# Kernel tuning notes

Measured on AMD Instinct MI355X. Metric: run time of the kernel, lower is better.

Reference implementation:

```python
import jax, jax.numpy as jnp
import numpy as np

V, N, K, D, H = 100000, 20000, 32, 256, 256


def setup_inputs() -> dict:
    key = jax.random.key(0)
    k1, k2, k3, k4, k5, k6 = jax.random.split(key, 6)
    return {
        "embed_table": jax.random.normal(k1, (V, D), dtype=jnp.float32),
        "node_ids": jax.random.randint(k2, (N,), 0, V, dtype=jnp.int64) if jax.config.jax_enable_x64 else jax.random.randint(k2, (N,), 0, V, dtype=jnp.int32),
        "nb_ids": jax.random.randint(k3, (N, K), 0, V, dtype=jnp.int32),
        "self_weight": jax.random.normal(k4, (D, H), dtype=jnp.float32) / np.sqrt(D),
        "nb_weight": jax.random.normal(k5, (D, H), dtype=jnp.float32) / np.sqrt(D),
        "bias": jax.random.normal(k6, (2 * H,), dtype=jnp.float32),
    }


def reference(embed_table, node_ids, nb_ids, self_weight, nb_weight, bias):
    # gather self embeddings: [N, D]
    self_attr = embed_table[node_ids]
    # gather sampled neighbor embeddings [N, K, D] and mean-pool over K
    nb_attr = jnp.mean(embed_table[nb_ids], axis=1)
    from_self = self_attr @ self_weight          # [N, H]
    from_nb = nb_attr @ nb_weight                # [N, H]
    out = jnp.concatenate((from_self, from_nb), axis=1) + bias  # concat combine
    return jax.nn.relu(out)
```

## Files before the change

### kernel.cpp

```cpp
#include <hip/hip_runtime.h>

#define VV 100000
#define NN 20000
#define KK 32
#define DD 256
#define HH 256
#define BN 16

typedef __attribute__((ext_vector_type(8))) short bf16x8;
typedef __attribute__((ext_vector_type(4))) float f32x4;

__device__ __forceinline__ ushort f2bf(float f) {
    uint u = __float_as_uint(f);
    return (ushort)((u + 0x7FFFu + ((u >> 16) & 1u)) >> 16);
}
__device__ __forceinline__ float bf2f(ushort u) {
    return __uint_as_float(((uint)u) << 16);
}

__global__ __launch_bounds__(256) void k_conv(
    const float* __restrict__ E, ushort* __restrict__ Eb)
{
    const size_t i = ((size_t)blockIdx.x * 256 + threadIdx.x) * 8;
    const f32x4 a = __builtin_nontemporal_load((const f32x4*)&E[i]);
    const f32x4 b = __builtin_nontemporal_load((const f32x4*)&E[i + 4]);
    bf16x8 v;
    v[0] = (short)f2bf(a.x); v[1] = (short)f2bf(a.y);
    v[2] = (short)f2bf(a.z); v[3] = (short)f2bf(a.w);
    v[4] = (short)f2bf(b.x); v[5] = (short)f2bf(b.y);
    v[6] = (short)f2bf(b.z); v[7] = (short)f2bf(b.w);
    *(bf16x8*)&Eb[i] = v;
}

__global__ __launch_bounds__(256) void k_prep_w(
    const float* __restrict__ Ws, const float* __restrict__ Wn,
    ushort* __restrict__ WT)
{
    __shared__ float t[64][65];
    const int tid = threadIdx.x;
    const float* src = (blockIdx.z == 0) ? Ws : Wn;
    ushort* dst = WT + (size_t)blockIdx.z * HH * DD;
    const int d0 = blockIdx.x * 64, h0 = blockIdx.y * 64;

    const int hl = tid & 63, dq = tid >> 6;
    #pragma unroll
    for (int i = 0; i < 16; ++i) {
        const int dl = dq * 16 + i;
        t[dl][hl] = src[(size_t)(d0 + dl) * HH + h0 + hl];
    }
    __syncthreads();
    const int dl = tid & 63, hq = tid >> 6;
    #pragma unroll
    for (int i = 0; i < 16; ++i) {
        const int h2 = hq * 16 + i;
        dst[(size_t)(h0 + h2) * DD + d0 + dl] = f2bf(t[dl][h2]);
    }
}

template<int EBF16>
__global__ __launch_bounds__(256, 4) void k_fused(
    const float*  __restrict__ Ef,
    const ushort* __restrict__ Eb,
    const int*    __restrict__ node_ids,
    const int*    __restrict__ nb_ids,
    const ushort* __restrict__ WT,
    const float*  __restrict__ bias,
    float*        __restrict__ out)
{
    __shared__ ushort As[BN][DD];
    __shared__ ushort An[BN][DD];
    const int tid  = threadIdx.x;
    const int wave = tid >> 6;
    const int lane = tid & 63;
    const int g0   = blockIdx.x * BN;

    if (EBF16) {
        const int sub = lane >> 5;
        const int l31 = lane & 31;
        const uint boff = (uint)l31 * 16;
        for (int n = wave; n < BN; n += 4) {
            const int g = g0 + n;
            const int base = g * KK;
            const uint swz = ((uint)(n & 7)) << 4;

            const int srow = node_ids[g];
            const bf16x8 sv = *(const bf16x8*)&Eb[((size_t)(uint)srow << 8) + l31 * 8];

            bf16x8 r[16];
            #pragma unroll
            for (int j = 0; j < 16; ++j) {
                const int rlo = nb_ids[base + 2 * j];
                const int rhi = nb_ids[base + 2 * j + 1];
                const int row = sub ? rhi : rlo;
                r[j] = *(const bf16x8*)&Eb[((size_t)(uint)row << 8) + l31 * 8];
            }
            float acc[8];
            #pragma unroll
            for (int e = 0; e < 8; ++e) acc[e] = 0.f;
            #pragma unroll
            for (int j = 0; j < 16; ++j) {
                #pragma unroll
                for (int e = 0; e < 8; ++e)
                    acc[e] += bf2f((ushort)r[j][e]);
            }
            #pragma unroll
            for (int e = 0; e < 8; ++e)
                acc[e] += __shfl_xor(acc[e], 32);

            const float inv = 1.0f / (float)KK;
            bf16x8 nv;
            #pragma unroll
            for (int e = 0; e < 8; ++e)
                nv[e] = (short)f2bf(acc[e] * inv);

            if (sub == 0) {
                *(bf16x8*)((char*)&As[n][0] + (boff ^ swz)) = sv;
            } else {
                *(bf16x8*)((char*)&An[n][0] + (boff ^ swz)) = nv;
            }
        }
    } else {
        for (int n = wave; n < BN; n += 4) {
            const int g = g0 + n;
            const int srow = node_ids[g];
            const uint swz  = ((uint)(n & 7)) << 4;
            const uint boff = (uint)lane * 8;
            const float4 s = *(const float4*)&Ef[(size_t)srow * DD + lane * 4];
            ushort4 sv = make_ushort4(f2bf(s.x), f2bf(s.y), f2bf(s.z), f2bf(s.w));
            float4 acc = make_float4(0.f, 0.f, 0.f, 0.f);
            #pragma unroll
            for (int k0 = 0; k0 < KK; k0 += 8) {
                float4 r[8];
                #pragma unroll
                for (int j = 0; j < 8; ++j) {
                    const int row = nb_ids[g * KK + k0 + j];
                    r[j] = *(const float4*)&Ef[(size_t)row * DD + lane * 4];
                }
                #pragma unroll
                for (int j = 0; j < 8; ++j) {
                    acc.x += r[j].x; acc.y += r[j].y;
                    acc.z += r[j].z; acc.w += r[j].w;
                }
            }
            const float inv = 1.0f / (float)KK;
            const ushort4 nv = make_ushort4(f2bf(acc.x * inv), f2bf(acc.y * inv),
                                            f2bf(acc.z * inv), f2bf(acc.w * inv));
            *(ushort4*)((char*)&As[n][0] + (boff ^ swz)) = sv;
            *(ushort4*)((char*)&An[n][0] + (boff ^ swz)) = nv;
        }
    }
    __syncthreads();

    const int half = wave >> 1;
    const int colq = (wave & 1) * 128;
    const int r16  = lane & 15;
    const int kg   = lane >> 4;
    const uint rswz = ((uint)(r16 & 7)) << 4;
    const char* Arow = (const char*)(half ? &An[r16][0] : &As[r16][0]);

    bf16x8 a[8];
    #pragma unroll
    for (int ks = 0; ks < 8; ++ks) {
        const uint off = (uint)(ks * 64 + kg * 16);
        a[ks] = *(const bf16x8*)(Arow + (off ^ rswz));
    }

    const ushort* Wb = WT + (size_t)half * HH * DD;
    f32x4 accs[8];
    #pragma unroll
    for (int ct = 0; ct < 8; ++ct) {
        const int c = colq + ct * 16 + r16;
        const ushort* Bb = Wb + (size_t)c * DD + kg * 8;
        f32x4 acc = {0.f, 0.f, 0.f, 0.f};
        #pragma unroll
        for (int ks = 0; ks < 8; ++ks) {
            const bf16x8 b = *(const bf16x8*)(Bb + ks * 32);
            acc = __builtin_amdgcn_mfma_f32_16x16x32_bf16(a[ks], b, acc, 0, 0, 0);
        }
        accs[ct] = acc;
    }

    #pragma unroll
    for (int ct = 0; ct < 8; ++ct) {
        const int cglob = half * HH + colq + ct * 16 + r16;
        const float bv = bias[cglob];
        #pragma unroll
        for (int r = 0; r < 4; ++r) {
            const float v = accs[ct][r] + bv;
            out[(size_t)(g0 + kg * 4 + r) * (2 * HH) + cglob] = v > 0.f ? v : 0.f;
        }
    }
}

__global__ __launch_bounds__(256, 4) void hetegraph_fused_kernel(
    const float* __restrict__ embed, const int* __restrict__ node_ids,
    const int* __restrict__ nb_ids, const float* __restrict__ Ws,
    const float* __restrict__ Wn, const float* __restrict__ bias,
    float* __restrict__ out)
{
    __shared__ float As[BN][DD];
    __shared__ float An[BN][DD];
    const int tid = threadIdx.x, wave = tid >> 6, lane = tid & 63;
    const int g0 = blockIdx.x * BN;
    for (int n = wave; n < BN; n += 4) {
        const int g = g0 + n;
        const int self_row = node_ids[g];
        const float4 s = *(const float4*)&embed[(size_t)self_row * DD + lane * 4];
        float4 acc = make_float4(0.f, 0.f, 0.f, 0.f);
        for (int k0 = 0; k0 < KK; k0 += 8) {
            float4 r[8];
            #pragma unroll
            for (int j = 0; j < 8; ++j) {
                const int row = nb_ids[g * KK + k0 + j];
                r[j] = *(const float4*)&embed[(size_t)row * DD + lane * 4];
            }
            #pragma unroll
            for (int j = 0; j < 8; ++j) {
                acc.x += r[j].x; acc.y += r[j].y; acc.z += r[j].z; acc.w += r[j].w;
            }
        }
        const float inv = 1.0f / (float)KK;
        *(float4*)&As[n][lane * 4] = s;
        float4 m = make_float4(acc.x * inv, acc.y * inv, acc.z * inv, acc.w * inv);
        *(float4*)&An[n][lane * 4] = m;
    }
    __syncthreads();
    const int h = tid;
    {
        float acc[BN];
        #pragma unroll
        for (int n = 0; n < BN; ++n) acc[n] = 0.f;
        for (int d0 = 0; d0 < DD; d0 += 4) {
            const float w0 = Ws[(d0+0)*HH+h], w1 = Ws[(d0+1)*HH+h];
            const float w2 = Ws[(d0+2)*HH+h], w3 = Ws[(d0+3)*HH+h];
            #pragma unroll
            for (int n = 0; n < BN; ++n) {
                const float4 a = *(const float4*)&As[n][d0];
                acc[n] = fmaf(a.x,w0,acc[n]); acc[n] = fmaf(a.y,w1,acc[n]);
                acc[n] = fmaf(a.z,w2,acc[n]); acc[n] = fmaf(a.w,w3,acc[n]);
            }
        }
        const float b = bias[h];
        #pragma unroll
        for (int n = 0; n < BN; ++n) {
            const float v = acc[n] + b;
            out[(size_t)(g0+n)*(2*HH) + h] = v > 0.f ? v : 0.f;
        }
    }
    {
        float acc[BN];
        #pragma unroll
        for (int n = 0; n < BN; ++n) acc[n] = 0.f;
        for (int d0 = 0; d0 < DD; d0 += 4) {
            const float w0 = Wn[(d0+0)*HH+h], w1 = Wn[(d0+1)*HH+h];
            const float w2 = Wn[(d0+2)*HH+h], w3 = Wn[(d0+3)*HH+h];
            #pragma unroll
            for (int n = 0; n < BN; ++n) {
                const float4 a = *(const float4*)&An[n][d0];
                acc[n] = fmaf(a.x,w0,acc[n]); acc[n] = fmaf(a.y,w1,acc[n]);
                acc[n] = fmaf(a.z,w2,acc[n]); acc[n] = fmaf(a.w,w3,acc[n]);
            }
        }
        const float b = bias[HH + h];
        #pragma unroll
        for (int n = 0; n < BN; ++n) {
            const float v = acc[n] + b;
            out[(size_t)(g0+n)*(2*HH) + HH + h] = v > 0.f ? v : 0.f;
        }
    }
}

extern "C" void kernel_launch(void* const* d_in, const int* in_sizes, int n_in,
                              void* d_out, int out_size, void* d_ws, size_t ws_size,
                              hipStream_t stream) {
    const float* embed    = (const float*)d_in[0];
    const int*   node_ids = (const int*)d_in[1];
    const int*   nb_ids   = (const int*)d_in[2];
    const float* Ws       = (const float*)d_in[3];
    const float* Wn       = (const float*)d_in[4];
    const float* bias     = (const float*)d_in[5];
    float*       out      = (float*)d_out;

    const size_t eb_bytes = (size_t)VV * DD * sizeof(ushort);
    const size_t wt_bytes = 2ull * HH * DD * sizeof(ushort);

    if (ws_size >= eb_bytes + wt_bytes) {
        ushort* Eb = (ushort*)d_ws;
        ushort* WT = (ushort*)((char*)d_ws + eb_bytes);
        k_conv<<<dim3(VV * DD / 2048), dim3(256), 0, stream>>>(embed, Eb);
        k_prep_w<<<dim3(DD / 64, HH / 64, 2), dim3(256), 0, stream>>>(Ws, Wn, WT);
        k_fused<1><<<dim3(NN / BN), dim3(256), 0, stream>>>(
            nullptr, Eb, node_ids, nb_ids, WT, bias, out);
    } else if (ws_size >= wt_bytes) {
        ushort* WT = (ushort*)d_ws;
        k_prep_w<<<dim3(DD / 64, HH / 64, 2), dim3(256), 0, stream>>>(Ws, Wn, WT);
        k_fused<0><<<dim3(NN / BN), dim3(256), 0, stream>>>(
            embed, nullptr, node_ids, nb_ids, WT, bias, out);
    } else {
        hetegraph_fused_kernel<<<dim3(NN / BN), dim3(256), 0, stream>>>(
            embed, node_ids, nb_ids, Ws, Wn, bias, out);
    }
}
```

Before: 108.3 us.

## Split fused gather+GEMM into gather and MFMA GEMM kernels with fragment-order layouts

Adds a new path that first gathers self and mean-pooled neighbor bf16 embeddings, one node per wave, and writes them to a workspace already arranged in MFMA operand-fragment order. A separate GEMM kernel then loads A and pre-swizzled weight fragments directly into registers and runs 16x16x32 bf16 MFMAs, with no LDS staging. The aim is to decouple the latency-bound gather from the compute phase, improve occupancy and remove LDS traffic and swizzling. The cost is an extra round-trip of the intermediate A through global memory and one more kernel launch.

Result: faster. 102.0 us (-5.8%).

```diff
diff --git a/kernel.cpp b/kernel.cpp
--- a/kernel.cpp
+++ b/kernel.cpp
@@ -32,6 +32,36 @@
     *(bf16x8*)&Eb[i] = v;
 }
 
+__global__ __launch_bounds__(256) void k_prep_wf(
+    const float* __restrict__ Ws, const float* __restrict__ Wn,
+    ushort* __restrict__ WTf)
+{
+    __shared__ float t[256][17];
+    const int tid = threadIdx.x;
+    const int h   = blockIdx.y;
+    const int tt  = blockIdx.x;
+    const float* src = h ? Wn : Ws;
+    const int h0 = tt * 16;
+    const int c = tid & 15, dr = tid >> 4;
+    #pragma unroll
+    for (int s = 0; s < 16; ++s) {
+        const int d = s * 16 + dr;
+        t[d][c] = src[(size_t)d * HH + h0 + c];
+    }
+    __syncthreads();
+    const int fl = tid & 63, w = tid >> 6;
+    const int r16 = fl & 15, kg = fl >> 4;
+    #pragma unroll
+    for (int p = 0; p < 2; ++p) {
+        const int ks = w + p * 4;
+        bf16x8 v;
+        #pragma unroll
+        for (int e = 0; e < 8; ++e)
+            v[e] = (short)f2bf(t[ks * 32 + kg * 8 + e][r16]);
+        *(bf16x8*)&WTf[(((size_t)(h * 16 + tt) * 8 + ks) * 64 + fl) * 8] = v;
+    }
+}
+
 __global__ __launch_bounds__(256) void k_prep_w(
     const float* __restrict__ Ws, const float* __restrict__ Wn,
     ushort* __restrict__ WT)
@@ -54,6 +84,97 @@
     for (int i = 0; i < 16; ++i) {
         const int h2 = hq * 16 + i;
         dst[(size_t)(h0 + h2) * DD + d0 + dl] = f2bf(t[dl][h2]);
+    }
+}
+
+__global__ __launch_bounds__(256, 4) void k_gatherf(
+    const ushort* __restrict__ Eb,
+    const int*    __restrict__ node_ids,
+    const int*    __restrict__ nb_ids,
+    ushort*       __restrict__ A)
+{
+    const int wv   = __builtin_amdgcn_readfirstlane((int)(threadIdx.x >> 6));
+    const int lane = threadIdx.x & 63;
+    const int sub  = lane >> 5;
+    const int l31  = lane & 31;
+    const int g    = blockIdx.x * 4 + wv;
+    const int base = g * KK;
+
+    const int srow = node_ids[g];
+    bf16x8 r[17];
+    r[0] = *(const bf16x8*)&Eb[((size_t)(uint)srow << 8) + l31 * 8];
+    #pragma unroll
+    for (int j = 1; j <= 16; ++j) {
+        const int rlo = nb_ids[base + j - 1];
+        const int rhi = nb_ids[base + j + 15];
+        const int row = sub ? rhi : rlo;
+        r[j] = *(const bf16x8*)&Eb[((size_t)(uint)row << 8) + l31 * 8];
+    }
+
+    float acc[8];
+    #pragma unroll
+    for (int e = 0; e < 8; ++e) acc[e] = 0.f;
+    #pragma unroll
+    for (int j = 1; j <= 16; ++j) {
+        #pragma unroll
+        for (int e = 0; e < 8; ++e)
+            acc[e] += bf2f((ushort)r[j][e]);
+    }
+    #pragma unroll
+    for (int e = 0; e < 8; ++e)
+        acc[e] += __shfl_xor(acc[e], 32);
+
+    const float inv = 1.0f / (float)KK;
+    bf16x8 nv;
+    #pragma unroll
+    for (int e = 0; e < 8; ++e)
+        nv[e] = (short)f2bf(acc[e] * inv);
+
+    const int tile = g >> 4, rr = g & 15;
+    const int ks = l31 >> 2, kgw = l31 & 3;
+    const size_t dst = (((size_t)(tile * 2 + sub) * 8 + ks) * 64 + kgw * 16 + rr) * 8;
+    *(bf16x8*)&A[dst] = sub ? nv : r[0];
+}
+
+__global__ __launch_bounds__(256, 4) void k_gemmf(
+    const ushort* __restrict__ A,
+    const ushort* __restrict__ WTf,
+    const float*  __restrict__ bias,
+    float*        __restrict__ out)
+{
+    const int wv   = __builtin_amdgcn_readfirstlane((int)(threadIdx.x >> 6));
+    const int lane = threadIdx.x & 63;
+    const int tile = blockIdx.x;
+    const int half = wv >> 1, qt = wv & 1;
+    const int r16 = lane & 15, kg = lane >> 4;
+
+    bf16x8 a[8];
+    #pragma unroll
+    for (int ks = 0; ks < 8; ++ks)
+        a[ks] = *(const bf16x8*)&A[(((size_t)(tile * 2 + half) * 8 + ks) * 64 + lane) * 8];
+
+    f32x4 accs[8];
+    #pragma unroll
+    for (int ct = 0; ct < 8; ++ct) {
+        const int t = qt * 8 + ct;
+        f32x4 acc = {0.f, 0.f, 0.f, 0.f};
+        #pragma unroll
+        for (int ks = 0; ks < 8; ++ks) {
+            const bf16x8 b = *(const bf16x8*)&WTf[(((size_t)(half * 16 + t) * 8 + ks) * 64 + lane) * 8];
+            acc = __builtin_amdgcn_mfma_f32_16x16x32_bf16(a[ks], b, acc, 0, 0, 0);
+        }
+        accs[ct] = acc;
+    }
+
+    #pragma unroll
+    for (int ct = 0; ct < 8; ++ct) {
+        const int cglob = half * HH + (qt * 8 + ct) * 16 + r16;
+        const float bv = bias[cglob];
+        #pragma unroll
+        for (int r = 0; r < 4; ++r) {
+            const float v = accs[ct][r] + bv;
+            out[(size_t)(tile * 16 + kg * 4 + r) * (2 * HH) + cglob] = v > 0.f ? v : 0.f;
+        }
     }
 }
 
@@ -82,10 +203,8 @@
             const int g = g0 + n;
             const int base = g * KK;
             const uint swz = ((uint)(n & 7)) << 4;
-
             const int srow = node_ids[g];
             const bf16x8 sv = *(const bf16x8*)&Eb[((size_t)(uint)srow << 8) + l31 * 8];
-
             bf16x8 r[16];
             #pragma unroll
             for (int j = 0; j < 16; ++j) {
@@ -106,13 +225,11 @@
             #pragma unroll
             for (int e = 0; e < 8; ++e)
                 acc[e] += __shfl_xor(acc[e], 32);
-
             const float inv = 1.0f / (float)KK;
             bf16x8 nv;
             #pragma unroll
             for (int e = 0; e < 8; ++e)
                 nv[e] = (short)f2bf(acc[e] * inv);
-
             if (sub == 0) {
                 *(bf16x8*)((char*)&As[n][0] + (boff ^ swz)) = sv;
             } else {
@@ -281,10 +398,20 @@
     const float* bias     = (const float*)d_in[5];
     float*       out      = (float*)d_out;
 
-    const size_t eb_bytes = (size_t)VV * DD * sizeof(ushort);
-    const size_t wt_bytes = 2ull * HH * DD * sizeof(ushort);
-
-    if (ws_size >= eb_bytes + wt_bytes) {
+    const size_t eb_bytes  = (size_t)VV * DD * sizeof(ushort);
+    const size_t wtf_bytes = 2ull * 16 * 8 * 64 * 8 * sizeof(ushort);
+    const size_t af_bytes  = (size_t)(NN / 16) * 2 * 8 * 64 * 8 * sizeof(ushort);
+    const size_t wt_bytes  = 2ull * HH * DD * sizeof(ushort);
+
+    if (ws_size >= eb_bytes + wtf_bytes + af_bytes) {
+        ushort* Eb  = (ushort*)d_ws;
+        ushort* WTf = (ushort*)((char*)d_ws + eb_bytes);
+        ushort* Af  = (ushort*)((char*)d_ws + eb_bytes + wtf_bytes);
+        k_prep_wf<<<dim3(16, 2), dim3(256), 0, stream>>>(Ws, Wn, WTf);
+        k_conv<<<dim3(VV * DD / 2048), dim3(256), 0, stream>>>(embed, Eb);
+        k_gatherf<<<dim3(NN / 4), dim3(256), 0, stream>>>(Eb, node_ids, nb_ids, Af);
+        k_gemmf<<<dim3(NN / 16), dim3(256), 0, stream>>>(Af, WTf, bias, out);
+    } else if (ws_size >= eb_bytes + wt_bytes) {
         ushort* Eb = (ushort*)d_ws;
         ushort* WT = (ushort*)((char*)d_ws + eb_bytes);
         k_conv<<<dim3(VV * DD / 2048), dim3(256), 0, stream>>>(embed, Eb);
```
